# Kernel optimization log

Hardware: AMD Instinct MI355X
Metric: run time of the kernel (lower is better)

## Reference

```python
import jax, jax.numpy as jnp
import numpy as np

N_NODES = 100000
N_EDGES = 1600000
D = 64  # edge feature dim == node hidden dim


def setup_inputs() -> dict:
    key = jax.random.key(0)
    k1, k2, k3, k4, k5, k6, k7 = jax.random.split(key, 7)
    edges = jax.random.normal(k1, (N_EDGES, D), dtype=jnp.float32)
    nodes = jax.random.normal(k2, (N_NODES, D), dtype=jnp.float32)
    receivers = jax.random.randint(k3, (N_EDGES,), 0, N_NODES, dtype=jnp.int32)
    s = 1.0 / np.sqrt(D)
    w_ih = jax.random.normal(k4, (3 * D, D), dtype=jnp.float32) * s
    w_hh = jax.random.normal(k5, (3 * D, D), dtype=jnp.float32) * s
    b_ih = jax.random.normal(k6, (3 * D,), dtype=jnp.float32) * s
    b_hh = jax.random.normal(k7, (3 * D,), dtype=jnp.float32) * s
    return {"edges": edges, "nodes": nodes, "receivers": receivers,
            "w_ih": w_ih, "w_hh": w_hh, "b_ih": b_ih, "b_hh": b_hh}


def reference(edges, nodes, receivers, w_ih, w_hh, b_ih, b_hh):
    # Scatter-aggregate edge features into receiver nodes: [N, D]
    aggr = jax.ops.segment_sum(edges, receivers, num_segments=nodes.shape[0])
    # GRU cell update (PyTorch/equinox gate order: reset, update, new)
    gi = aggr @ w_ih.T + b_ih      # [N, 3D]
    gh = nodes @ w_hh.T + b_hh     # [N, 3D]
    i_r, i_z, i_n = jnp.split(gi, 3, axis=-1)
    h_r, h_z, h_n = jnp.split(gh, 3, axis=-1)
    r = jax.nn.sigmoid(i_r + h_r)
    z = jax.nn.sigmoid(i_z + h_z)
    n = jnp.tanh(i_n + r * h_n)
    new_nodes = (1.0 - z) * n + z * nodes
    return new_nodes
```

## Files before the change

kernel.cpp:

```cpp
#include <hip/hip_runtime.h>
#include <math.h>

#define N_NODES_C 100000
#define N_EDGES_C 1600000
#define DIM 64
#define G3 192
#define SCAN_B 1024
#define N_SCAN_BLOCKS ((N_NODES_C + SCAN_B - 1) / SCAN_B)

typedef short bf16x8 __attribute__((ext_vector_type(8)));
typedef float f32x4 __attribute__((ext_vector_type(4)));

__device__ __forceinline__ unsigned short bf16_rne(float f) {
    unsigned int u = __float_as_uint(f);
    return (unsigned short)((u + 0x7FFFu + ((u >> 16) & 1u)) >> 16);
}

__device__ __forceinline__ void split2(float f0, float f1,
                                       unsigned int& hi, unsigned int& lo) {
    const unsigned int u0 = __float_as_uint(f0);
    const unsigned int u1 = __float_as_uint(f1);
    const float l0 = f0 - __uint_as_float(u0 & 0xFFFF0000u);
    const float l1 = f1 - __uint_as_float(u1 & 0xFFFF0000u);
    hi = (u0 >> 16) | ((u1 >> 16) << 16);
    lo = (unsigned int)bf16_rne(l0) | ((unsigned int)bf16_rne(l1) << 16);
}

__device__ __forceinline__ float bf16f(unsigned short h) {
    return __uint_as_float(((unsigned int)h) << 16);
}

__global__ void hist_kernel(const int* __restrict__ receivers,
                            int* __restrict__ count,
                            int* __restrict__ rank) {
    int e = blockIdx.x * blockDim.x + threadIdx.x;
    if (e >= N_EDGES_C) return;
    int r = receivers[e];
    rank[e] = __hip_atomic_fetch_add(&count[r], 1,
                                     __ATOMIC_RELAXED, __HIP_MEMORY_SCOPE_AGENT);
}

__global__ void scan1_kernel(const int* __restrict__ count,
                             int* __restrict__ offsets,
                             int* __restrict__ bsums) {
    __shared__ int wsum[16];
    const int gid  = blockIdx.x * SCAN_B + threadIdx.x;
    const int lane = threadIdx.x & 63;
    const int wv   = threadIdx.x >> 6;
    int c = (gid < N_NODES_C) ? count[gid] : 0;
    int x = c;
    #pragma unroll
    for (int o = 1; o < 64; o <<= 1) {
        int v = __shfl_up(x, o);
        if (lane >= o) x += v;
    }
    if (lane == 63) wsum[wv] = x;
    __syncthreads();
    if (wv == 0) {
        int s = (lane < 16) ? wsum[lane] : 0;
        #pragma unroll
        for (int o = 1; o < 16; o <<= 1) {
            int v = __shfl_up(s, o);
            if (lane >= o) s += v;
        }
        if (lane < 16) wsum[lane] = s;
    }
    __syncthreads();
    int woff = (wv == 0) ? 0 : wsum[wv - 1];
    if (gid < N_NODES_C) offsets[gid] = woff + x - c;
    if (threadIdx.x == SCAN_B - 1) bsums[blockIdx.x] = wsum[15];
}

__global__ void scan2_kernel(int* __restrict__ bsums) {
    __shared__ int w0tot;
    const int i    = threadIdx.x;
    const int lane = threadIdx.x & 63;
    const int wv   = threadIdx.x >> 6;
    int c = (i < N_SCAN_BLOCKS) ? bsums[i] : 0;
    int x = c;
    #pragma unroll
    for (int o = 1; o < 64; o <<= 1) {
        int v = __shfl_up(x, o);
        if (lane >= o) x += v;
    }
    if (wv == 0 && lane == 63) w0tot = x;
    __syncthreads();
    int add = (wv == 1) ? w0tot : 0;
    if (i < N_SCAN_BLOCKS) bsums[i] = add + x - c;
}

__global__ void permw_kernel(const int* __restrict__ receivers,
                             const int* __restrict__ offsets,
                             const int* __restrict__ bsums,
                             const int* __restrict__ rank,
                             int* __restrict__ perm) {
    int e = blockIdx.x * blockDim.x + threadIdx.x;
    if (e >= N_EDGES_C) return;
    int r = receivers[e];
    perm[offsets[r] + bsums[r >> 10] + rank[e]] = e;
}

__global__ void prep_w_kernel(const float* __restrict__ w_ih,
                              const float* __restrict__ w_hh,
                              unsigned short* __restrict__ img_w) {
    const int ci  = blockIdx.x * 256 + threadIdx.x;
    if (ci >= 3072) return;
    const int mat = ci / 1536;
    const int rem = ci - mat * 1536;
    const int col = rem >> 3;
    const int ch  = rem & 7;
    const float* w = mat ? w_hh : w_ih;
    const float4 f0 = *reinterpret_cast<const float4*>(w + col * 64 + ch * 8);
    const float4 f1 = *reinterpret_cast<const float4*>(w + col * 64 + ch * 8 + 4);
    unsigned int hi[4], lo[4];
    split2(f0.x, f0.y, hi[0], lo[0]);
    split2(f0.z, f0.w, hi[1], lo[1]);
    split2(f1.x, f1.y, hi[2], lo[2]);
    split2(f1.z, f1.w, hi[3], lo[3]);
    unsigned short* dst = img_w + mat * 24576 + col * 64 + ((ch ^ (col & 7)) << 3);
    *reinterpret_cast<uint4*>(dst)         = make_uint4(hi[0], hi[1], hi[2], hi[3]);
    *reinterpret_cast<uint4*>(dst + 12288) = make_uint4(lo[0], lo[1], lo[2], lo[3]);
}

__global__ void prep_nodes_kernel(const float* __restrict__ nodes,
                                  unsigned short* __restrict__ n_hi,
                                  unsigned short* __restrict__ n_lo) {
    const int t = blockIdx.x * 256 + threadIdx.x;
    if (t >= N_NODES_C * 16) return;
    const int row = t >> 4;
    const int cc  = t & 15;
    const float4 f = *reinterpret_cast<const float4*>(nodes + (size_t)row * 64 + cc * 4);
    unsigned int h0, l0, h1, l1;
    split2(f.x, f.y, h0, l0);
    split2(f.z, f.w, h1, l1);
    const int addr = row * 64 + (((cc >> 1) ^ (row & 7)) << 3) + ((cc & 1) << 2);
    *reinterpret_cast<uint2*>(n_hi + addr) = make_uint2(h0, h1);
    *reinterpret_cast<uint2*>(n_lo + addr) = make_uint2(l0, l1);
}

__global__ __launch_bounds__(256)
void gather_kernel(const float* __restrict__ edges,
                   const int* __restrict__ perm,
                   const int* __restrict__ offsets,
                   const int* __restrict__ bsums,
                   const int* __restrict__ count,
                   unsigned short* __restrict__ a_hi,
                   unsigned short* __restrict__ a_lo) {
    const int w    = (blockIdx.x << 2) | (threadIdx.x >> 6);
    const int lane = threadIdx.x & 63;
    if (w >= N_NODES_C) return;
    const int g    = lane >> 4;
    const int c4   = (lane & 15) << 2;
    const int start = offsets[w] + bsums[w >> 10];
    const int cnt   = count[w];

    float4 a0 = make_float4(0.f, 0.f, 0.f, 0.f);
    float4 a1 = a0, a2 = a0, a3 = a0;

    int done = 0;
    while (done < cnt) {
        const int pv  = perm[start + min(done + lane, cnt - 1)];
        const int lim = min(cnt - done, 64);
        const int nq  = (lim + 15) >> 4;
        for (int q = 0; q < nq; ++q) {
            const int rbase = q << 4;
            #pragma unroll
            for (int b = 0; b < 4; ++b) {
                const int rr  = rbase + (b << 2) + g;
                const int src = min(rr, lim - 1);
                const int e   = __shfl(pv, src);
                const float4 v = *reinterpret_cast<const float4*>(
                    edges + (size_t)e * DIM + c4);
                const float m = (rr < lim) ? 1.f : 0.f;
                if (b == 0) { a0.x += v.x*m; a0.y += v.y*m; a0.z += v.z*m; a0.w += v.w*m; }
                if (b == 1) { a1.x += v.x*m; a1.y += v.y*m; a1.z += v.z*m; a1.w += v.w*m; }
                if (b == 2) { a2.x += v.x*m; a2.y += v.y*m; a2.z += v.z*m; a2.w += v.w*m; }
                if (b == 3) { a3.x += v.x*m; a3.y += v.y*m; a3.z += v.z*m; a3.w += v.w*m; }
            }
        }
        done += 64;
    }

    float4 s;
    s.x = (a0.x + a1.x) + (a2.x + a3.x);
    s.y = (a0.y + a1.y) + (a2.y + a3.y);
    s.z = (a0.z + a1.z) + (a2.z + a3.z);
    s.w = (a0.w + a1.w) + (a2.w + a3.w);
    #pragma unroll
    for (int m = 16; m <= 32; m <<= 1) {
        s.x += __shfl_xor(s.x, m);
        s.y += __shfl_xor(s.y, m);
        s.z += __shfl_xor(s.z, m);
        s.w += __shfl_xor(s.w, m);
    }
    if (lane < 16) {
        const int l15 = lane;
        unsigned int h0, l0, h1, l1;
        split2(s.x, s.y, h0, l0);
        split2(s.z, s.w, h1, l1);
        const int addr = w * 64 + ((((l15) >> 1) ^ (w & 7)) << 3) + ((l15 & 1) << 2);
        *reinterpret_cast<uint2*>(a_hi + addr) = make_uint2(h0, h1);
        *reinterpret_cast<uint2*>(a_lo + addr) = make_uint2(l0, l1);
    }
}

__global__ __launch_bounds__(256, 2)
void gru_mfma_kernel(const unsigned short* __restrict__ img_w,
                     const unsigned short* __restrict__ aggr_hi,
                     const unsigned short* __restrict__ aggr_lo,
                     const unsigned short* __restrict__ nodes_hi,
                     const unsigned short* __restrict__ nodes_lo,
                     const float* __restrict__ b_ih,
                     const float* __restrict__ b_hh,
                     float* __restrict__ out) {
    __shared__ __align__(16) unsigned short s_w[24576];
    __shared__ __align__(16) unsigned short s_a[8192];

    const int tid  = threadIdx.x;
    const int lane = tid & 63;
    const int wave = tid >> 6;
    const int nb   = blockIdx.x * 64;
    const int l15  = lane & 15;
    const int lg   = lane >> 4;
    const int arow = (wave << 4) + l15;

    float bir[4], biz[4], bin_[4], bhr[4], bhz[4], bhn[4];
    #pragma unroll
    for (int t = 0; t < 4; ++t) {
        const int o = l15 + (t << 4);
        bir[t] = b_ih[o]; biz[t] = b_ih[64 + o]; bin_[t] = b_ih[128 + o];
        bhr[t] = b_hh[o]; bhz[t] = b_hh[64 + o]; bhn[t] = b_hh[128 + o];
    }

    f32x4 accA[12], accB[12];
    #pragma unroll
    for (int ct = 0; ct < 12; ++ct) { accA[ct] = (f32x4)(0.f); accB[ct] = (f32x4)(0.f); }

    {
        const uint4* wsrc = reinterpret_cast<const uint4*>(img_w);
        uint4* wdst = reinterpret_cast<uint4*>(s_w);
        #pragma unroll
        for (int i = 0; i < 12; ++i) wdst[tid + i * 256] = wsrc[tid + i * 256];
        const uint4* hsrc = reinterpret_cast<const uint4*>(aggr_hi + (size_t)nb * 64);
        const uint4* lsrc = reinterpret_cast<const uint4*>(aggr_lo + (size_t)nb * 64);
        uint4* adst = reinterpret_cast<uint4*>(s_a);
        #pragma unroll
        for (int i = 0; i < 2; ++i) {
            adst[tid + i * 256]       = hsrc[tid + i * 256];
            adst[512 + tid + i * 256] = lsrc[tid + i * 256];
        }
    }
    __syncthreads();

    #pragma unroll
    for (int kt = 0; kt < 2; ++kt) {
        const int ach = ((kt * 4 + lg) ^ (arow & 7)) << 3;
        const bf16x8 ahi = *reinterpret_cast<const bf16x8*>(&s_a[arow * 64 + ach]);
        const bf16x8 alo = *reinterpret_cast<const bf16x8*>(&s_a[4096 + arow * 64 + ach]);
        #pragma unroll
        for (int ct = 0; ct < 12; ++ct) {
            const int col = ct * 16 + l15;
            const int sw  = ((kt * 4 + lg) ^ (col & 7)) << 3;
            const bf16x8 bhi = *reinterpret_cast<const bf16x8*>(&s_w[col * 64 + sw]);
            const bf16x8 blo = *reinterpret_cast<const bf16x8*>(&s_w[12288 + col * 64 + sw]);
            accA[ct] = __builtin_amdgcn_mfma_f32_16x16x32_bf16(ahi, bhi, accA[ct], 0, 0, 0);
            accA[ct] = __builtin_amdgcn_mfma_f32_16x16x32_bf16(alo, bhi, accA[ct], 0, 0, 0);
            accA[ct] = __builtin_amdgcn_mfma_f32_16x16x32_bf16(ahi, blo, accA[ct], 0, 0, 0);
        }
    }
    __syncthreads();

    {
        const uint4* wsrc = reinterpret_cast<const uint4*>(img_w + 24576);
        uint4* wdst = reinterpret_cast<uint4*>(s_w);
        #pragma unroll
        for (int i = 0; i < 12; ++i) wdst[tid + i * 256] = wsrc[tid + i * 256];
        const uint4* hsrc = reinterpret_cast<const uint4*>(nodes_hi + (size_t)nb * 64);
        const uint4* lsrc = reinterpret_cast<const uint4*>(nodes_lo + (size_t)nb * 64);
        uint4* adst = reinterpret_cast<uint4*>(s_a);
        #pragma unroll
        for (int i = 0; i < 2; ++i) {
            adst[tid + i * 256]       = hsrc[tid + i * 256];
            adst[512 + tid + i * 256] = lsrc[tid + i * 256];
        }
    }
    __syncthreads();

    #pragma unroll
    for (int kt = 0; kt < 2; ++kt) {
        const int ach = ((kt * 4 + lg) ^ (arow & 7)) << 3;
        const bf16x8 ahi = *reinterpret_cast<const bf16x8*>(&s_a[arow * 64 + ach]);
        const bf16x8 alo = *reinterpret_cast<const bf16x8*>(&s_a[4096 + arow * 64 + ach]);
        #pragma unroll
        for (int ct = 0; ct < 12; ++ct) {
            const int col = ct * 16 + l15;
            const int sw  = ((kt * 4 + lg) ^ (col & 7)) << 3;
            const bf16x8 bhi = *reinterpret_cast<const bf16x8*>(&s_w[col * 64 + sw]);
            const bf16x8 blo = *reinterpret_cast<const bf16x8*>(&s_w[12288 + col * 64 + sw]);
            accB[ct] = __builtin_amdgcn_mfma_f32_16x16x32_bf16(ahi, bhi, accB[ct], 0, 0, 0);
            accB[ct] = __builtin_amdgcn_mfma_f32_16x16x32_bf16(alo, bhi, accB[ct], 0, 0, 0);
            accB[ct] = __builtin_amdgcn_mfma_f32_16x16x32_bf16(ahi, blo, accB[ct], 0, 0, 0);
        }
    }

    #pragma unroll
    for (int t = 0; t < 4; ++t) {
        #pragma unroll
        for (int rg = 0; rg < 4; ++rg) {
            const int rr   = (wave << 4) + (lg << 2) + rg;
            const int node = nb + rr;
            const int o    = l15 + (t << 4);
            const float ir = accA[t][rg]     + bir[t];
            const float iz = accA[4 + t][rg] + biz[t];
            const float inn= accA[8 + t][rg] + bin_[t];
            const float hr = accB[t][rg]     + bhr[t];
            const float hz = accB[4 + t][rg] + bhz[t];
            const float hn = accB[8 + t][rg] + bhn[t];
            const float r = 1.f / (1.f + __expf(-(ir + hr)));
            const float z = 1.f / (1.f + __expf(-(iz + hz)));
            float tt = inn + r * hn;
            tt = fminf(fmaxf(tt, -15.f), 15.f);
            const float e2 = __expf(2.f * tt);
            const float ng = (e2 - 1.f) / (e2 + 1.f);
            const int idx = rr * 64 + (((o >> 3) ^ (rr & 7)) << 3) + (o & 7);
            const float h = bf16f(s_a[idx]) + bf16f(s_a[4096 + idx]);
            if (node < N_NODES_C)
                out[(size_t)node * 64 + o] = (1.f - z) * ng + z * h;
        }
    }
}

extern "C" void kernel_launch(void* const* d_in, const int* in_sizes, int n_in,
                              void* d_out, int out_size, void* d_ws, size_t ws_size,
                              hipStream_t stream) {
    const float* edges     = (const float*)d_in[0];
    const float* nodes     = (const float*)d_in[1];
    const int*   receivers = (const int*)d_in[2];
    const float* w_ih      = (const float*)d_in[3];
    const float* w_hh      = (const float*)d_in[4];
    const float* b_ih      = (const float*)d_in[5];
    const float* b_hh      = (const float*)d_in[6];
    float* out = (float*)d_out;

    int* ws      = (int*)d_ws;
    int* count   = ws;
    int* offsets = ws + N_NODES_C;
    int* rank    = ws + 2 * N_NODES_C;
    int* perm    = rank + N_EDGES_C;
    int* bsums   = perm + N_EDGES_C;
    unsigned short* img_w   = (unsigned short*)(ws + 3400192);
    unsigned short* aggr_hi = img_w + 4 * 12288;
    unsigned short* aggr_lo = aggr_hi + (size_t)N_NODES_C * 64;
    unsigned short* n_hi    = aggr_lo + (size_t)N_NODES_C * 64;
    unsigned short* n_lo    = n_hi    + (size_t)N_NODES_C * 64;

    hipMemsetAsync(count, 0, N_NODES_C * sizeof(int), stream);

    prep_w_kernel<<<12, 256, 0, stream>>>(w_ih, w_hh, img_w);
    prep_nodes_kernel<<<(N_NODES_C * 16 + 255) / 256, 256, 0, stream>>>(nodes, n_hi, n_lo);

    hist_kernel<<<(N_EDGES_C + 255) / 256, 256, 0, stream>>>(receivers, count, rank);
    scan1_kernel<<<N_SCAN_BLOCKS, SCAN_B, 0, stream>>>(count, offsets, bsums);
    scan2_kernel<<<1, 128, 0, stream>>>(bsums);
    permw_kernel<<<(N_EDGES_C + 255) / 256, 256, 0, stream>>>(receivers, offsets, bsums, rank, perm);

    gather_kernel<<<(N_NODES_C + 3) / 4, 256, 0, stream>>>(
        edges, perm, offsets, bsums, count, aggr_hi, aggr_lo);

    gru_mfma_kernel<<<(N_NODES_C + 63) / 64, 256, 0, stream>>>(
        img_w, aggr_hi, aggr_lo, n_hi, n_lo, b_ih, b_hh, out);
}
```

Measured before the change: 249.4 us.

## Gather four consecutive nodes per wavefront with fully unrolled 64-edge batches

Measured after the change: 253.6 us. About the same (+1.7%).

```diff
diff --git a/kernel.cpp b/kernel.cpp
--- a/kernel.cpp
+++ b/kernel.cpp
@@ -139,68 +139,90 @@
 }
 
 __global__ __launch_bounds__(256)
-void gather_kernel(const float* __restrict__ edges,
-                   const int* __restrict__ perm,
-                   const int* __restrict__ offsets,
-                   const int* __restrict__ bsums,
-                   const int* __restrict__ count,
-                   unsigned short* __restrict__ a_hi,
-                   unsigned short* __restrict__ a_lo) {
-    const int w    = (blockIdx.x << 2) | (threadIdx.x >> 6);
+void gather4_kernel(const float* __restrict__ edges,
+                    const int* __restrict__ perm,
+                    const int* __restrict__ offsets,
+                    const int* __restrict__ bsums,
+                    const int* __restrict__ count,
+                    unsigned short* __restrict__ a_hi,
+                    unsigned short* __restrict__ a_lo) {
+    const int wgid = (blockIdx.x << 2) | (threadIdx.x >> 6);
+    const int n0   = wgid << 2;
+    if (n0 >= N_NODES_C) return;
     const int lane = threadIdx.x & 63;
-    if (w >= N_NODES_C) return;
     const int g    = lane >> 4;
     const int c4   = (lane & 15) << 2;
-    const int start = offsets[w] + bsums[w >> 10];
-    const int cnt   = count[w];
-
-    float4 a0 = make_float4(0.f, 0.f, 0.f, 0.f);
-    float4 a1 = a0, a2 = a0, a3 = a0;
+
+    const int off0 = offsets[n0] + bsums[n0 >> 10];
+    const int c0 = count[n0], c1 = count[n0 + 1];
+    const int c2 = count[n0 + 2], c3 = count[n0 + 3];
+    const int b1 = c0, b2 = c0 + c1, b3 = c0 + c1 + c2;
+    const int total = b3 + c3;
+
+    float4 acc0 = make_float4(0.f, 0.f, 0.f, 0.f);
+    float4 acc1 = acc0, acc2 = acc0, acc3 = acc0;
 
     int done = 0;
-    while (done < cnt) {
-        const int pv  = perm[start + min(done + lane, cnt - 1)];
-        const int lim = min(cnt - done, 64);
-        const int nq  = (lim + 15) >> 4;
-        for (int q = 0; q < nq; ++q) {
-            const int rbase = q << 4;
+    while (done < total) {
+        const int lim = min(total - done, 64);
+        const int pv  = perm[off0 + done + min(lane, lim - 1)];
+        float4 v[16];
+        #pragma unroll
+        for (int q = 0; q < 4; ++q) {
             #pragma unroll
             for (int b = 0; b < 4; ++b) {
-                const int rr  = rbase + (b << 2) + g;
-                const int src = min(rr, lim - 1);
-                const int e   = __shfl(pv, src);
-                const float4 v = *reinterpret_cast<const float4*>(
+                const int rr = (q << 4) + (b << 2) + g;
+                const int e  = __shfl(pv, min(rr, lim - 1));
+                v[q * 4 + b] = *reinterpret_cast<const float4*>(
                     edges + (size_t)e * DIM + c4);
-                const float m = (rr < lim) ? 1.f : 0.f;
-                if (b == 0) { a0.x += v.x*m; a0.y += v.y*m; a0.z += v.z*m; a0.w += v.w*m; }
-                if (b == 1) { a1.x += v.x*m; a1.y += v.y*m; a1.z += v.z*m; a1.w += v.w*m; }
-                if (b == 2) { a2.x += v.x*m; a2.y += v.y*m; a2.z += v.z*m; a2.w += v.w*m; }
-                if (b == 3) { a3.x += v.x*m; a3.y += v.y*m; a3.z += v.z*m; a3.w += v.w*m; }
             }
         }
+        #pragma unroll
+        for (int q = 0; q < 4; ++q) {
+            #pragma unroll
+            for (int b = 0; b < 4; ++b) {
+                const int rr = (q << 4) + (b << 2) + g;
+                const int rg = done + rr;
+                const bool valid = rr < lim;
+                const float m0 = (valid & (rg < b1)) ? 1.f : 0.f;
+                const float m1 = (valid & (rg >= b1) & (rg < b2)) ? 1.f : 0.f;
+                const float m2 = (valid & (rg >= b2) & (rg < b3)) ? 1.f : 0.f;
+                const float m3 = (valid & (rg >= b3)) ? 1.f : 0.f;
+                const float4 vv = v[q * 4 + b];
+                acc0.x += vv.x * m0; acc0.y += vv.y * m0; acc0.z += vv.z * m0; acc0.w += vv.w * m0;
+                acc1.x += vv.x * m1; acc1.y += vv.y * m1; acc1.z += vv.z * m1; acc1.w += vv.w * m1;
+                acc2.x += vv.x * m2; acc2.y += vv.y * m2; acc2.z += vv.z * m2; acc2.w += vv.w * m2;
+                acc3.x += vv.x * m3; acc3.y += vv.y * m3; acc3.z += vv.z * m3; acc3.w += vv.w * m3;
+            }
+        }
         done += 64;
     }
 
-    float4 s;
-    s.x = (a0.x + a1.x) + (a2.x + a3.x);
-    s.y = (a0.y + a1.y) + (a2.y + a3.y);
-    s.z = (a0.z + a1.z) + (a2.z + a3.z);
-    s.w = (a0.w + a1.w) + (a2.w + a3.w);
     #pragma unroll
     for (int m = 16; m <= 32; m <<= 1) {
-        s.x += __shfl_xor(s.x, m);
-        s.y += __shfl_xor(s.y, m);
-        s.z += __shfl_xor(s.z, m);
-        s.w += __shfl_xor(s.w, m);
-    }
+        acc0.x += __shfl_xor(acc0.x, m); acc0.y += __shfl_xor(acc0.y, m);
+        acc0.z += __shfl_xor(acc0.z, m); acc0.w += __shfl_xor(acc0.w, m);
+        acc1.x += __shfl_xor(acc1.x, m); acc1.y += __shfl_xor(acc1.y, m);
+        acc1.z += __shfl_xor(acc1.z, m); acc1.w += __shfl_xor(acc1.w, m);
+        acc2.x += __shfl_xor(acc2.x, m); acc2.y += __shfl_xor(acc2.y, m);
+        acc2.z += __shfl_xor(acc2.z, m); acc2.w += __shfl_xor(acc2.w, m);
+        acc3.x += __shfl_xor(acc3.x, m); acc3.y += __shfl_xor(acc3.y, m);
+        acc3.z += __shfl_xor(acc3.z, m); acc3.w += __shfl_xor(acc3.w, m);
+    }
+
     if (lane < 16) {
         const int l15 = lane;
-        unsigned int h0, l0, h1, l1;
-        split2(s.x, s.y, h0, l0);
-        split2(s.z, s.w, h1, l1);
-        const int addr = w * 64 + ((((l15) >> 1) ^ (w & 7)) << 3) + ((l15 & 1) << 2);
-        *reinterpret_cast<uint2*>(a_hi + addr) = make_uint2(h0, h1);
-        *reinterpret_cast<uint2*>(a_lo + addr) = make_uint2(l0, l1);
+        const float4 accs[4] = {acc0, acc1, acc2, acc3};
+        #pragma unroll
+        for (int j = 0; j < 4; ++j) {
+            const int w = n0 + j;
+            unsigned int h0, l0, h1, l1;
+            split2(accs[j].x, accs[j].y, h0, l0);
+            split2(accs[j].z, accs[j].w, h1, l1);
+            const int addr = w * 64 + (((l15 >> 1) ^ (w & 7)) << 3) + ((l15 & 1) << 2);
+            *reinterpret_cast<uint2*>(a_hi + addr) = make_uint2(h0, h1);
+            *reinterpret_cast<uint2*>(a_lo + addr) = make_uint2(l0, l1);
+        }
     }
 }
 
@@ -364,7 +386,7 @@
     scan2_kernel<<<1, 128, 0, stream>>>(bsums);
     permw_kernel<<<(N_EDGES_C + 255) / 256, 256, 0, stream>>>(receivers, offsets, bsums, rank, perm);
 
-    gather_kernel<<<(N_NODES_C + 3) / 4, 256, 0, stream>>>(
+    gather4_kernel<<<(N_NODES_C + 15) / 16, 256, 0, stream>>>(
         edges, perm, offsets, bsums, count, aggr_hi, aggr_lo);
 
     gru_mfma_kernel<<<(N_NODES_C + 63) / 64, 256, 0, stream>>>(
```
